# Optimization experiments

Hardware: AMD Instinct MI355X
Metric: run time of the kernel (lower is better)

Reference implementation:

```python
import jax, jax.numpy as jnp
import numpy as np

EPS = 1e-5  # nn.BatchNorm2d default eps


def _cbs(x, w, g, b, m, v):
    # Conv(k=1, bias=False) + BatchNorm2d(inference) + SiLU
    y = jnp.einsum('bchw,oc->bohw', x, w)
    s = (g * jax.lax.rsqrt(v + EPS))[None, :, None, None]
    y = (y - m[None, :, None, None]) * s + b[None, :, None, None]
    return y * jax.nn.sigmoid(y)


def setup_inputs():
    key = jax.random.key(0)
    B, D, H, W = 1, 256, 80, 80
    C = D // 2
    ks = jax.random.split(key, 20)
    r = lambda i, shape, sc=1.0: jax.random.normal(ks[i], shape, dtype=jnp.float32) * sc
    oC, oD = jnp.ones((C,), jnp.float32), jnp.ones((D,), jnp.float32)
    zC, zD = jnp.zeros((C,), jnp.float32), jnp.zeros((D,), jnp.float32)
    return {
        'x': r(0, (B, D, H, W)),
        'w1': r(1, (C, D), 0.05), 'g1': oC, 'b1': zC, 'm1': zC, 'v1': oC,
        'w2': r(2, (D, C), 0.05), 'g2': oD, 'b2': zD, 'm2': zD, 'v2': oD,
        'w3': r(3, (D, C), 0.05), 'g3': oD, 'b3': zD, 'm3': zD, 'v3': oD,
        'wq': r(4, (C, C), 0.05), 'bq': r(5, (C,), 0.01),
        'wk': r(6, (C, C), 0.05), 'bk': r(7, (C,), 0.01),
        'wv': r(8, (C, C), 0.05), 'bv': r(9, (C,), 0.01),
        'wp': r(10, (C, C), 0.05), 'bp': r(11, (C,), 0.01),
        'rel_h': r(12, (1, C, H, 1)), 'rel_w': r(13, (1, C, 1, W)),
        'ef_h': r(14, (1, C, H, 1)), 'ef_w': r(15, (1, C, 1, W)),
    }


def reference(x, w1, g1, b1, m1, v1, w2, g2, b2, m2, v2, w3, g3, b3, m3, v3,
              wq, bq, wk, bk, wv, bv, wp, bp, rel_h, rel_w, ef_h, ef_w):
    x1 = _cbs(x, w1, g1, b1, m1, v1)            # [B, C, H, W]
    B, C, H, W = x1.shape
    HW = H * W
    proj = lambda w, b: (jnp.einsum('bchw,oc->bohw', x1, w)
                         + b[None, :, None, None]).reshape(B, C, HW)
    q = proj(wq, bq)
    k = proj(wk, bk)
    v = proj(wv, bv)
    p = proj(wp, bp)
    # content-content + content-position attention branch
    cp = (rel_h + rel_w).reshape(C, HW)          # [C, HW]
    cc = jnp.einsum('bci,bcj->bij', q, k)        # [B, HW, HW]
    cpos = jnp.einsum('ci,bcj->bij', cp, q)      # [B, HW, HW]
    attn = jax.nn.softmax(cc + cpos, axis=-1)
    # out1[b,c,i] = sum_j v[b,c,j] * attn[b,i,j]  (bmm(v, attn^T))
    out1 = jnp.einsum('bcj,bij->bci', v, attn).reshape(B, C, H, W)
    # extra positional branch (valid because B == 1)
    ef = (ef_h + ef_w).reshape(B, C, HW)         # [1, C, HW]
    ce = jnp.einsum('bci,bcj->bij', p, ef)       # [B, HW, HW]
    eng = jax.nn.softmax(ce, axis=-1)
    out2 = jnp.einsum('bcj,bij->bci', ef, eng).reshape(B, C, H, W)
    return x + _cbs(out1, w2, g2, b2, m2, v2) + _cbs(out2, w3, g3, b3, m3, v3)
```

## Files before the change

kernel.cpp:

```cpp
#include <hip/hip_runtime.h>


typedef unsigned short u16;
typedef __attribute__((ext_vector_type(8))) short bf16x8;
typedef __attribute__((ext_vector_type(4))) float f32x4;
typedef __attribute__((ext_vector_type(4))) unsigned int u32x4;

#define HW 6400
#define BN_EPS 1e-5f

__device__ __forceinline__ u16 f2b(float f) {
  unsigned u = __float_as_uint(f);
  u += 0x7fffu + ((u >> 16) & 1u);
  return (u16)(u >> 16);
}
__device__ __forceinline__ unsigned pack2(float a, float b) {
  return (unsigned)f2b(a) | ((unsigned)f2b(b) << 16);
}
__device__ __forceinline__ f32x4 MFMA(bf16x8 a, bf16x8 b, f32x4 c) {
  return __builtin_amdgcn_mfma_f32_16x16x32_bf16(a, b, c, 0, 0, 0);
}
__device__ __forceinline__ float silu_f(float y) {
  return y / (1.0f + __expf(-y));
}
__device__ __forceinline__ bf16x8 pack8(f32x4 lo, f32x4 hi, float sc) {
  union { bf16x8 v; uint4 u; } r;
  r.u.x = pack2(lo[0] * sc, lo[1] * sc);
  r.u.y = pack2(lo[2] * sc, lo[3] * sc);
  r.u.z = pack2(hi[0] * sc, hi[1] * sc);
  r.u.w = pack2(hi[2] * sc, hi[3] * sc);
  return r.v;
}
__device__ __forceinline__ void gload_lds16(const u16* src, u16* dst) {
  __builtin_amdgcn_global_load_lds(
      (const __attribute__((address_space(1))) void*)src,
      (__attribute__((address_space(3))) void*)dst, 16, 0, 0);
}

__global__ void prep_all(
    const float* __restrict__ rel_h, const float* __restrict__ rel_w,
    const float* __restrict__ ef_h, const float* __restrict__ ef_w,
    const float* __restrict__ w1, const float* __restrict__ g1, const float* __restrict__ b1,
    const float* __restrict__ m1, const float* __restrict__ v1,
    const float* __restrict__ w2, const float* __restrict__ g2, const float* __restrict__ b2,
    const float* __restrict__ m2, const float* __restrict__ v2,
    const float* __restrict__ w3, const float* __restrict__ g3, const float* __restrict__ b3,
    const float* __restrict__ m3, const float* __restrict__ v3,
    const float* __restrict__ wq, const float* __restrict__ bq,
    const float* __restrict__ wk, const float* __restrict__ bk,
    const float* __restrict__ wv, const float* __restrict__ bv,
    const float* __restrict__ wp, const float* __restrict__ bp,
    u16* __restrict__ LT,
    u16* __restrict__ w1b, float* __restrict__ b1e,
    u16* __restrict__ Wcat, float* __restrict__ bcat,
    u16* __restrict__ w2b, float* __restrict__ b2e,
    u16* __restrict__ w3b, float* __restrict__ b3e,
    u16* __restrict__ efhT, u16* __restrict__ efwT,
    u16* __restrict__ efhB, u16* __restrict__ efwB,
    float* __restrict__ lbuf)
{
  const int b = blockIdx.x;
  const int t = threadIdx.x;
  if (b < 80) {
    const int h = b;
    const int c0 = (t & 63) * 2;
    const float rh0 = rel_h[c0 * 80 + h], rh1 = rel_h[(c0 + 1) * 80 + h];
    for (int wcol = (t >> 6); wcol < 80; wcol += 4) {
      const int i = h * 80 + wcol;
      float rw0 = rel_w[c0 * 80 + wcol], rw1 = rel_w[(c0 + 1) * 80 + wcol];
      *(unsigned*)&LT[(size_t)i * 256 + 128 + c0] = pack2(rh0 + rw0, rh1 + rw1);
    }
  } else if (b < 144) {
    const int tid = (b - 80) * 256 + t;
    const int stride = 64 * 256;
    for (int idx = tid; idx < 128 * 256; idx += stride) {
      int o = idx >> 8;
      float s = g1[o] * rsqrtf(v1[o] + BN_EPS);
      w1b[idx] = f2b(w1[idx] * s);
    }
    for (int idx = tid; idx < 128; idx += stride) {
      float s = g1[idx] * rsqrtf(v1[idx] + BN_EPS);
      b1e[idx] = b1[idx] - m1[idx] * s;
    }
    for (int idx = tid; idx < 4 * 128 * 128; idx += stride) {
      int which = idx >> 14, r = idx & 16383;
      const float* src = which == 0 ? wq : which == 1 ? wk : which == 2 ? wv : wp;
      Wcat[idx] = f2b(src[r]);
    }
    for (int idx = tid; idx < 512; idx += stride) {
      int which = idx >> 7, r = idx & 127;
      const float* src = which == 0 ? bq : which == 1 ? bk : which == 2 ? bv : bp;
      bcat[idx] = src[r];
    }
    for (int idx = tid; idx < 256 * 128; idx += stride) {
      int o = idx >> 7;
      float s2 = g2[o] * rsqrtf(v2[o] + BN_EPS);
      w2b[idx] = f2b(w2[idx] * s2);
      float s3 = g3[o] * rsqrtf(v3[o] + BN_EPS);
      w3b[idx] = f2b(w3[idx] * s3);
    }
    for (int idx = tid; idx < 256; idx += stride) {
      float s2 = g2[idx] * rsqrtf(v2[idx] + BN_EPS);
      b2e[idx] = b2[idx] - m2[idx] * s2;
      float s3 = g3[idx] * rsqrtf(v3[idx] + BN_EPS);
      b3e[idx] = b3[idx] - m3[idx] * s3;
    }
    for (int idx = tid; idx < 80 * 128; idx += stride) {
      int hj = idx >> 7, c = idx & 127;
      efhT[idx] = f2b(ef_h[c * 80 + hj]);
      efwT[idx] = f2b(ef_w[c * 80 + hj]);
    }
    for (int idx = tid; idx < 128 * 96; idx += stride) {
      int c = idx / 96, hj = idx % 96;
      efhB[idx] = hj < 80 ? f2b(ef_h[c * 80 + hj]) : (u16)0;
      efwB[idx] = hj < 80 ? f2b(ef_w[c * 80 + hj]) : (u16)0;
    }
  } else {
    const int tid = (b - 144) * 256 + t;
    const int stride = 32 * 256;
    for (int idx = tid; idx < HW / 4; idx += stride)
      ((f32x4*)lbuf)[idx] = (f32x4){0.f, 0.f, 0.f, 0.f};
  }
}

__global__ __launch_bounds__(256) void front_k(
    const float* __restrict__ x,
    const u16* __restrict__ w1b, const float* __restrict__ b1e,
    const u16* __restrict__ Wcat, const float* __restrict__ bcat,
    u16* __restrict__ LT, u16* __restrict__ RT, u16* __restrict__ Vv,
    u16* __restrict__ pT)
{
  __shared__ __align__(16) float xs[16][260];
  __shared__ __align__(16) u16 tr[16][136];
  const int t = threadIdx.x, lane = t & 63, w = t >> 6, jl = lane & 15, q = lane >> 4;
  const int i0 = blockIdx.x * 16;

#pragma unroll
  for (int pp = 0; pp < 4; ++pp) {
    const int p = w * 4 + pp;
    const int ch = p * 16 + (lane >> 2);
    const int ii = (lane & 3) * 4;
    f32x4 v = *(const f32x4*)(x + (size_t)ch * HW + i0 + ii);
    xs[ii][ch] = v[0]; xs[ii + 1][ch] = v[1];
    xs[ii + 2][ch] = v[2]; xs[ii + 3][ch] = v[3];
  }
  __syncthreads();

  bf16x8 afr[8];
#pragma unroll
  for (int ks = 0; ks < 8; ++ks) {
    f32x4 va = *(const f32x4*)&xs[jl][ks * 32 + q * 8];
    f32x4 vb = *(const f32x4*)&xs[jl][ks * 32 + q * 8 + 4];
    afr[ks] = pack8(va, vb, 1.0f);
  }
  f32x4 acc[2];
#pragma unroll
  for (int nn = 0; nn < 2; ++nn) acc[nn] = (f32x4){0.f, 0.f, 0.f, 0.f};
#pragma unroll
  for (int ks = 0; ks < 8; ++ks)
#pragma unroll
    for (int nn = 0; nn < 2; ++nn) {
      const int nf = w * 2 + nn;
      bf16x8 b = *(const bf16x8*)(w1b + (size_t)(nf * 16 + jl) * 256 + ks * 32 + q * 8);
      acc[nn] = MFMA(afr[ks], b, acc[nn]);
    }
#pragma unroll
  for (int nn = 0; nn < 2; ++nn) {
    const int c = (w * 2 + nn) * 16 + jl;
    const float bias = b1e[c];
#pragma unroll
    for (int r = 0; r < 4; ++r)
      tr[q * 4 + r][c] = f2b(silu_f(acc[nn][r] + bias));
  }
  __syncthreads();
  bf16x8 xa[4];
#pragma unroll
  for (int ks = 0; ks < 4; ++ks)
    xa[ks] = *(const bf16x8*)&tr[jl][ks * 32 + q * 8];

#pragma unroll
  for (int nc = 0; nc < 4; ++nc) {
    f32x4 a2[2];
#pragma unroll
    for (int nn = 0; nn < 2; ++nn) a2[nn] = (f32x4){0.f, 0.f, 0.f, 0.f};
#pragma unroll
    for (int ks = 0; ks < 4; ++ks)
#pragma unroll
      for (int nn = 0; nn < 2; ++nn) {
        const int nf = w * 2 + nn;
        bf16x8 b = *(const bf16x8*)(Wcat + (size_t)(nc * 128 + nf * 16 + jl) * 128 + ks * 32 + q * 8);
        a2[nn] = MFMA(xa[ks], b, a2[nn]);
      }
    if (nc == 2) {
#pragma unroll
      for (int nn = 0; nn < 2; ++nn) {
        const int c = (w * 2 + nn) * 16 + jl;
        const float bias = bcat[256 + c];
        uint2 pk;
        pk.x = pack2(a2[nn][0] + bias, a2[nn][1] + bias);
        pk.y = pack2(a2[nn][2] + bias, a2[nn][3] + bias);
        *(uint2*)(Vv + (size_t)c * HW + i0 + q * 4) = pk;
      }
    } else {
      __syncthreads();
#pragma unroll
      for (int nn = 0; nn < 2; ++nn) {
        const int c = (w * 2 + nn) * 16 + jl;
        const float bias = bcat[nc * 128 + c];
#pragma unroll
        for (int r = 0; r < 4; ++r)
          tr[q * 4 + r][c] = f2b(a2[nn][r] + bias);
      }
      __syncthreads();
#pragma unroll
      for (int rr = 0; rr < 4; ++rr) {
        const int r = w * 4 + rr;
        unsigned val = *(const unsigned*)&tr[r][lane * 2];
        const size_t row = (size_t)(i0 + r);
        if (nc == 0) {
          *(unsigned*)(LT + row * 256 + lane * 2) = val;
          *(unsigned*)(RT + row * 256 + 128 + lane * 2) = val;
        } else if (nc == 1) {
          *(unsigned*)(RT + row * 256 + lane * 2) = val;
        } else {
          *(unsigned*)(pT + row * 128 + lane * 2) = val;
        }
      }
    }
  }
}

__global__ __launch_bounds__(512, 2) void fused_attn(
    const u16* __restrict__ LT,
    const u16* __restrict__ RT,
    const u16* __restrict__ Vv,
    float* __restrict__ Opart,
    float* __restrict__ lv)
{
  __shared__ __align__(1024) u16 Rs[2][128 * 128];
  __shared__ __align__(1024) u16 Ts[2][64 * 128];
  const int t = threadIdx.x, lane = t & 63, w = t >> 6, jl = lane & 15, q = lane >> 4;
  const int bid = blockIdx.x;
  const int jp = bid / 50, it = bid % 50;
  const int wi = w & 1, wj = w >> 1;
  const int i0w = it * 128 + wi * 64;
  u16* Tw = Ts[wi];

  bf16x8 afr[4][8];
#pragma unroll
  for (int mt = 0; mt < 4; ++mt)
#pragma unroll
    for (int l = 0; l < 8; ++l)
      afr[mt][l] = *(const bf16x8*)(LT + (size_t)(i0w + mt * 16 + jl) * 256 + l * 32 + q * 8);

  f32x4 o[4][2];
#pragma unroll
  for (int mt = 0; mt < 4; ++mt)
#pragma unroll
    for (int cf = 0; cf < 2; ++cf) o[mt][cf] = (f32x4){0.f, 0.f, 0.f, 0.f};
  float lacc[4] = {0.f, 0.f, 0.f, 0.f};

  auto stage = [&](int jj) {
#pragma unroll
    for (int k = 0; k < 8; ++k) {
      const int b = k >> 2, cl = k & 3;
      const int cc = w * 4 + cl;
      const int jr = cc * 4 + (lane >> 4);
      const int cp = lane & 15;
      const int ch = (cp & ~7) | ((cp ^ jr) & 7);
      gload_lds16(RT + (size_t)(jj + jr) * 256 + b * 128 + ch * 8,
                  Rs[b] + (cc << 9));
    }
  };

  stage(jp * 640);

  for (int stp = 0; stp < 5; ++stp) {
    const int jj = jp * 640 + stp * 128;

    f32x4 s[2][4];
#pragma unroll
    for (int nf = 0; nf < 2; ++nf)
#pragma unroll
      for (int mt = 0; mt < 4; ++mt) s[nf][mt] = (f32x4){0.f, 0.f, 0.f, 0.f};

    __syncthreads();

#pragma unroll
    for (int h = 0; h < 2; ++h)
#pragma unroll
      for (int nf = 0; nf < 2; ++nf) {
        const int row = wj * 32 + nf * 16 + jl;
#pragma unroll
        for (int l = 0; l < 4; ++l) {
          const int ch = (l * 4 + q) ^ (jl & 7);
          bf16x8 b = *(const bf16x8*)(Rs[h] + row * 128 + ch * 8);
          s[nf][0] = MFMA(b, afr[0][h * 4 + l], s[nf][0]);
          s[nf][1] = MFMA(b, afr[1][h * 4 + l], s[nf][1]);
          s[nf][2] = MFMA(b, afr[2][h * 4 + l], s[nf][2]);
          s[nf][3] = MFMA(b, afr[3][h * 4 + l], s[nf][3]);
        }
      }
    __syncthreads();
    if (stp < 4) stage(jj + 128);

#pragma unroll
    for (int nf = 0; nf < 2; ++nf)
#pragma unroll
      for (int mt = 0; mt < 4; ++mt)
#pragma unroll
        for (int r = 0; r < 4; ++r) {
          float p = __expf(s[nf][mt][r]);
          s[nf][mt][r] = p;
          lacc[mt] += p;
        }

#pragma unroll
    for (int mt = 0; mt < 4; ++mt)
#pragma unroll
      for (int nf = 0; nf < 2; ++nf) {
        const int row = mt * 16 + jl;
        const int cs = (wj * 8 + nf * 4 + q) ^ ((jl & 7) << 2);
        uint2 pk;
        pk.x = pack2(s[nf][mt][0], s[nf][mt][1]);
        pk.y = pack2(s[nf][mt][2], s[nf][mt][3]);
        *(uint2*)(Tw + row * 128 + cs * 4) = pk;
      }
    __syncthreads();

#pragma unroll
    for (int ks2 = 0; ks2 < 4; ++ks2) {
      bf16x8 bv0 = *(const bf16x8*)(Vv + (size_t)(wj * 32 + jl) * HW + jj + ks2 * 32 + q * 8);
      bf16x8 bv1 = *(const bf16x8*)(Vv + (size_t)(wj * 32 + 16 + jl) * HW + jj + ks2 * 32 + q * 8);
      const int cb = (ks2 * 8 + q * 2) ^ ((jl & 7) << 2);
#pragma unroll
      for (int mt = 0; mt < 4; ++mt) {
        bf16x8 pa = *(const bf16x8*)(Tw + (mt * 16 + jl) * 128 + cb * 4);
        o[mt][0] = MFMA(pa, bv0, o[mt][0]);
        o[mt][1] = MFMA(pa, bv1, o[mt][1]);
      }
    }
  }

#pragma unroll
  for (int mt = 0; mt < 4; ++mt) {
    float rsum = lacc[mt];
    rsum += __shfl_xor(rsum, 16);
    rsum += __shfl_xor(rsum, 32);
    if (lane < 16)
      atomicAdd(&lv[i0w + mt * 16 + jl], rsum);
  }
#pragma unroll
  for (int mt = 0; mt < 4; ++mt) {
    const int ib = i0w + mt * 16 + q * 4;
#pragma unroll
    for (int cf = 0; cf < 2; ++cf) {
      const int c = wj * 32 + cf * 16 + jl;
#pragma unroll
      for (int r = 0; r < 4; ++r)
        Opart[((size_t)(ib + r) * 10 + jp) * 128 + c] = o[mt][cf][r];
    }
  }
}

__global__ __launch_bounds__(256) void final2(
    const u16* __restrict__ pT,
    const u16* __restrict__ efhT, const u16* __restrict__ efwT,
    const u16* __restrict__ efhB, const u16* __restrict__ efwB,
    const float* __restrict__ Opart,
    const float* __restrict__ lv,
    const u16* __restrict__ w2b, const float* __restrict__ b2e,
    const u16* __restrict__ w3b, const float* __restrict__ b3e,
    const float* __restrict__ x, float* __restrict__ outp)
{
  __shared__ __align__(16) u16 eAs[64][104];
  __shared__ __align__(16) u16 eBs[64][104];
  __shared__ float sAL[64], sBL[64];
  __shared__ __align__(16) u16 T2[64][136];
  const int t = threadIdx.x, lane = t & 63, w = t >> 6, jl = lane & 15, q = lane >> 4;
  const int i0 = blockIdx.x * 64;
  const int nc = blockIdx.y;
  const int rowA = i0 + w * 16 + jl;
  const int iloc = w * 16 + jl;

  {
    bf16x8 pfr[4];
#pragma unroll
    for (int l = 0; l < 4; ++l)
      pfr[l] = *(const bf16x8*)(pT + (size_t)rowA * 128 + l * 32 + q * 8);
    f32x4 sa[5], sb[5];
#pragma unroll
    for (int nf = 0; nf < 5; ++nf) {
      sa[nf] = (f32x4){0.f, 0.f, 0.f, 0.f};
      sb[nf] = (f32x4){0.f, 0.f, 0.f, 0.f};
    }
#pragma unroll
    for (int nf = 0; nf < 5; ++nf) {
      const int row = nf * 16 + jl;
#pragma unroll
      for (int l = 0; l < 4; ++l) {
        bf16x8 eh = *(const bf16x8*)(efhT + (size_t)row * 128 + l * 32 + q * 8);
        bf16x8 ew = *(const bf16x8*)(efwT + (size_t)row * 128 + l * 32 + q * 8);
        sa[nf] = MFMA(eh, pfr[l], sa[nf]);
        sb[nf] = MFMA(ew, pfr[l], sb[nf]);
      }
    }
    float ra = 0.f, rb = 0.f;
#pragma unroll
    for (int nf = 0; nf < 5; ++nf) {
      float ea[4], eb[4];
#pragma unroll
      for (int r = 0; r < 4; ++r) {
        ea[r] = __expf(sa[nf][r]); ra += ea[r];
        eb[r] = __expf(sb[nf][r]); rb += eb[r];
      }
      uint2 pa, pb;
      pa.x = pack2(ea[0], ea[1]); pa.y = pack2(ea[2], ea[3]);
      pb.x = pack2(eb[0], eb[1]); pb.y = pack2(eb[2], eb[3]);
      *(uint2*)&eAs[iloc][nf * 16 + q * 4] = pa;
      *(uint2*)&eBs[iloc][nf * 16 + q * 4] = pb;
    }
    *(uint2*)&eAs[iloc][80 + q * 4] = (uint2){0u, 0u};
    *(uint2*)&eBs[iloc][80 + q * 4] = (uint2){0u, 0u};
    ra += __shfl_xor(ra, 16); ra += __shfl_xor(ra, 32);
    rb += __shfl_xor(rb, 16); rb += __shfl_xor(rb, 32);
    if (lane < 16) { sAL[iloc] = ra; sBL[iloc] = rb; }
  }
  __syncthreads();

  {
    bf16x8 fa[3], fb[3];
#pragma unroll
    for (int l = 0; l < 3; ++l) {
      fa[l] = *(const bf16x8*)&eAs[iloc][l * 32 + q * 8];
      fb[l] = *(const bf16x8*)&eBs[iloc][l * 32 + q * 8];
    }
    f32x4 oU[8], oW[8];
#pragma unroll
    for (int nf = 0; nf < 8; ++nf) {
      oU[nf] = (f32x4){0.f, 0.f, 0.f, 0.f};
      oW[nf] = (f32x4){0.f, 0.f, 0.f, 0.f};
    }
#pragma unroll
    for (int l = 0; l < 3; ++l)
#pragma unroll
      for (int nf = 0; nf < 8; ++nf) {
        bf16x8 bh = *(const bf16x8*)(efhB + (size_t)(nf * 16 + jl) * 96 + l * 32 + q * 8);
        bf16x8 bw = *(const bf16x8*)(efwB + (size_t)(nf * 16 + jl) * 96 + l * 32 + q * 8);
        oU[nf] = MFMA(fa[l], bh, oU[nf]);
        oW[nf] = MFMA(fb[l], bw, oW[nf]);
      }
    float ia[4], iw[4];
#pragma unroll
    for (int r = 0; r < 4; ++r) {
      ia[r] = 1.0f / sAL[w * 16 + q * 4 + r];
      iw[r] = 1.0f / sBL[w * 16 + q * 4 + r];
    }
#pragma unroll
    for (int nf = 0; nf < 8; ++nf)
#pragma unroll
      for (int r = 0; r < 4; ++r)
        T2[w * 16 + q * 4 + r][nf * 16 + jl] =
            f2b(oU[nf][r] * ia[r] + oW[nf][r] * iw[r]);
  }
  __syncthreads();

  const float inv1 = 1.0f / lv[rowA];
  const float* OrBase = Opart + (size_t)rowA * 10 * 128;
  f32x4 a1[8], a2[8];
#pragma unroll
  for (int nf = 0; nf < 8; ++nf) {
    a1[nf] = (f32x4){0.f, 0.f, 0.f, 0.f};
    a2[nf] = (f32x4){0.f, 0.f, 0.f, 0.f};
  }
#pragma unroll
  for (int ks = 0; ks < 4; ++ks) {
    f32x4 s1a = (f32x4){0.f, 0.f, 0.f, 0.f};
    f32x4 s1b = (f32x4){0.f, 0.f, 0.f, 0.f};
#pragma unroll
    for (int p = 0; p < 10; ++p) {
      const float* Or = OrBase + p * 128;
      s1a += *(const f32x4*)(Or + ks * 32 + q * 8);
      s1b += *(const f32x4*)(Or + ks * 32 + q * 8 + 4);
    }
    bf16x8 fa1 = pack8(s1a, s1b, inv1);
    bf16x8 fa2 = *(const bf16x8*)&T2[w * 16 + jl][ks * 32 + q * 8];
#pragma unroll
    for (int nf = 0; nf < 8; ++nf) {
      bf16x8 b2f = *(const bf16x8*)(w2b + (size_t)(nc * 128 + nf * 16 + jl) * 128 + ks * 32 + q * 8);
      bf16x8 b3f = *(const bf16x8*)(w3b + (size_t)(nc * 128 + nf * 16 + jl) * 128 + ks * 32 + q * 8);
      a1[nf] = MFMA(fa1, b2f, a1[nf]);
      a2[nf] = MFMA(fa2, b3f, a2[nf]);
    }
  }
#pragma unroll
  for (int nf = 0; nf < 8; ++nf) {
    const int d = nc * 128 + nf * 16 + jl;
    const float bb2 = b2e[d], bb3 = b3e[d];
    const size_t base = (size_t)d * HW + i0 + w * 16 + q * 4;
    f32x4 xv = *(const f32x4*)(x + base);
    f32x4 rv;
#pragma unroll
    for (int r = 0; r < 4; ++r)
      rv[r] = xv[r] + silu_f(a1[nf][r] + bb2) + silu_f(a2[nf][r] + bb3);
    *(f32x4*)(outp + base) = rv;
  }
}

extern "C" void kernel_launch(void* const* d_in, const int* in_sizes, int n_in,
                              void* d_out, int out_size, void* d_ws, size_t ws_size,
                              hipStream_t stream)
{
  (void)in_sizes; (void)n_in; (void)out_size; (void)ws_size;
  const float* x   = (const float*)d_in[0];
  const float* w1  = (const float*)d_in[1];
  const float* g1  = (const float*)d_in[2];
  const float* b1  = (const float*)d_in[3];
  const float* m1  = (const float*)d_in[4];
  const float* v1  = (const float*)d_in[5];
  const float* w2  = (const float*)d_in[6];
  const float* g2  = (const float*)d_in[7];
  const float* b2  = (const float*)d_in[8];
  const float* m2  = (const float*)d_in[9];
  const float* v2  = (const float*)d_in[10];
  const float* w3  = (const float*)d_in[11];
  const float* g3  = (const float*)d_in[12];
  const float* b3  = (const float*)d_in[13];
  const float* m3  = (const float*)d_in[14];
  const float* v3  = (const float*)d_in[15];
  const float* wq  = (const float*)d_in[16];
  const float* bq  = (const float*)d_in[17];
  const float* wk  = (const float*)d_in[18];
  const float* bk  = (const float*)d_in[19];
  const float* wv  = (const float*)d_in[20];
  const float* bv  = (const float*)d_in[21];
  const float* wp  = (const float*)d_in[22];
  const float* bp  = (const float*)d_in[23];
  const float* rel_h = (const float*)d_in[24];
  const float* rel_w = (const float*)d_in[25];
  const float* ef_h  = (const float*)d_in[26];
  const float* ef_w  = (const float*)d_in[27];
  float* outp = (float*)d_out;

  char* ws = (char*)d_ws;
  size_t off = 0;
  auto alloc = [&](size_t bytes) -> void* {
    void* p = ws + off;
    off += (bytes + 511) & ~(size_t)511;
    return p;
  };
  u16* LT    = (u16*)alloc((size_t)HW * 256 * 2);
  u16* RT    = (u16*)alloc((size_t)HW * 256 * 2);
  u16* pT    = (u16*)alloc((size_t)HW * 128 * 2);
  u16* Vv    = (u16*)alloc((size_t)HW * 128 * 2);
  float* Opart = (float*)alloc((size_t)HW * 10 * 128 * 4);
  float* lbuf  = (float*)alloc((size_t)HW * 4);
  u16* w1b   = (u16*)alloc(128 * 256 * 2);
  float* b1e = (float*)alloc(128 * 4);
  u16* Wcat  = (u16*)alloc(512 * 128 * 2);
  float* bcat = (float*)alloc(512 * 4);
  u16* w2b   = (u16*)alloc(256 * 128 * 2);
  float* b2e = (float*)alloc(256 * 4);
  u16* w3b   = (u16*)alloc(256 * 128 * 2);
  float* b3e = (float*)alloc(256 * 4);
  u16* efhT  = (u16*)alloc(80 * 128 * 2);
  u16* efwT  = (u16*)alloc(80 * 128 * 2);
  u16* efhB  = (u16*)alloc(128 * 96 * 2);
  u16* efwB  = (u16*)alloc(128 * 96 * 2);

  prep_all<<<176, 256, 0, stream>>>(rel_h, rel_w, ef_h, ef_w,
                                    w1, g1, b1, m1, v1, w2, g2, b2, m2, v2,
                                    w3, g3, b3, m3, v3, wq, bq, wk, bk, wv, bv, wp, bp,
                                    LT, w1b, b1e, Wcat, bcat, w2b, b2e, w3b, b3e,
                                    efhT, efwT, efhB, efwB, lbuf);
  front_k<<<400, 256, 0, stream>>>(x, w1b, b1e, Wcat, bcat, LT, RT, Vv, pT);
  fused_attn<<<500, 512, 0, stream>>>(LT, RT, Vv, Opart, lbuf);
  final2<<<dim3(100, 2), 256, 0, stream>>>(pT, efhT, efwT, efhB, efwB,
                                           Opart, lbuf, w2b, b2e, w3b, b3e,
                                           x, outp);
}
```

Measured before the change: 240.8 us.

## Factor positional score term into separable h/w tables, halve attention K dimension

The content-position term cp^T q is split into rel_h and rel_w parts. Their products with q are precomputed in front_k as two 80xHW float tables (Ap, Bp) and added before the exp. This halves the reduction depth of the score MFMA (128 instead of 256) and halves the LT/RT storage and the RT staging traffic. Staging is also turned into true double buffering with one barrier per step. The cost is two extra fp32 table loads per score element in the attention loop and the extra table writes in front_k.

```diff
diff --git a/kernel.cpp b/kernel.cpp
--- a/kernel.cpp
+++ b/kernel.cpp
@@ -50,28 +50,19 @@
     const float* __restrict__ wk, const float* __restrict__ bk,
     const float* __restrict__ wv, const float* __restrict__ bv,
     const float* __restrict__ wp, const float* __restrict__ bp,
-    u16* __restrict__ LT,
     u16* __restrict__ w1b, float* __restrict__ b1e,
     u16* __restrict__ Wcat, float* __restrict__ bcat,
     u16* __restrict__ w2b, float* __restrict__ b2e,
     u16* __restrict__ w3b, float* __restrict__ b3e,
     u16* __restrict__ efhT, u16* __restrict__ efwT,
     u16* __restrict__ efhB, u16* __restrict__ efwB,
+    u16* __restrict__ rhT, u16* __restrict__ rwT,
     float* __restrict__ lbuf)
 {
   const int b = blockIdx.x;
   const int t = threadIdx.x;
-  if (b < 80) {
-    const int h = b;
-    const int c0 = (t & 63) * 2;
-    const float rh0 = rel_h[c0 * 80 + h], rh1 = rel_h[(c0 + 1) * 80 + h];
-    for (int wcol = (t >> 6); wcol < 80; wcol += 4) {
-      const int i = h * 80 + wcol;
-      float rw0 = rel_w[c0 * 80 + wcol], rw1 = rel_w[(c0 + 1) * 80 + wcol];
-      *(unsigned*)&LT[(size_t)i * 256 + 128 + c0] = pack2(rh0 + rw0, rh1 + rw1);
-    }
-  } else if (b < 144) {
-    const int tid = (b - 80) * 256 + t;
+  if (b < 64) {
+    const int tid = b * 256 + t;
     const int stride = 64 * 256;
     for (int idx = tid; idx < 128 * 256; idx += stride) {
       int o = idx >> 8;
@@ -109,6 +100,8 @@
       int hj = idx >> 7, c = idx & 127;
       efhT[idx] = f2b(ef_h[c * 80 + hj]);
       efwT[idx] = f2b(ef_w[c * 80 + hj]);
+      rhT[idx]  = f2b(rel_h[c * 80 + hj]);
+      rwT[idx]  = f2b(rel_w[c * 80 + hj]);
     }
     for (int idx = tid; idx < 128 * 96; idx += stride) {
       int c = idx / 96, hj = idx % 96;
@@ -116,7 +109,7 @@
       efwB[idx] = hj < 80 ? f2b(ef_w[c * 80 + hj]) : (u16)0;
     }
   } else {
-    const int tid = (b - 144) * 256 + t;
+    const int tid = (b - 64) * 256 + t;
     const int stride = 32 * 256;
     for (int idx = tid; idx < HW / 4; idx += stride)
       ((f32x4*)lbuf)[idx] = (f32x4){0.f, 0.f, 0.f, 0.f};
@@ -127,8 +120,10 @@
     const float* __restrict__ x,
     const u16* __restrict__ w1b, const float* __restrict__ b1e,
     const u16* __restrict__ Wcat, const float* __restrict__ bcat,
+    const u16* __restrict__ rhT, const u16* __restrict__ rwT,
     u16* __restrict__ LT, u16* __restrict__ RT, u16* __restrict__ Vv,
-    u16* __restrict__ pT)
+    u16* __restrict__ pT,
+    float* __restrict__ Ap, float* __restrict__ Bp)
 {
   __shared__ __align__(16) float xs[16][260];
   __shared__ __align__(16) u16 tr[16][136];
@@ -218,12 +213,34 @@
         unsigned val = *(const unsigned*)&tr[r][lane * 2];
         const size_t row = (size_t)(i0 + r);
         if (nc == 0) {
-          *(unsigned*)(LT + row * 256 + lane * 2) = val;
-          *(unsigned*)(RT + row * 256 + 128 + lane * 2) = val;
+          *(unsigned*)(LT + row * 128 + lane * 2) = val;
         } else if (nc == 1) {
-          *(unsigned*)(RT + row * 256 + lane * 2) = val;
+          *(unsigned*)(RT + row * 128 + lane * 2) = val;
         } else {
           *(unsigned*)(pT + row * 128 + lane * 2) = val;
+        }
+      }
+      if (nc == 0) {
+        bf16x8 qf[4];
+#pragma unroll
+        for (int ks = 0; ks < 4; ++ks)
+          qf[ks] = *(const bf16x8*)&tr[jl][ks * 32 + q * 8];
+        for (int nf = w; nf < 5; nf += 4) {
+          f32x4 aa = (f32x4){0.f, 0.f, 0.f, 0.f};
+          f32x4 bb = (f32x4){0.f, 0.f, 0.f, 0.f};
+#pragma unroll
+          for (int ks = 0; ks < 4; ++ks) {
+            bf16x8 rh = *(const bf16x8*)(rhT + (size_t)(nf * 16 + jl) * 128 + ks * 32 + q * 8);
+            bf16x8 rw = *(const bf16x8*)(rwT + (size_t)(nf * 16 + jl) * 128 + ks * 32 + q * 8);
+            aa = MFMA(rh, qf[ks], aa);
+            bb = MFMA(rw, qf[ks], bb);
+          }
+#pragma unroll
+          for (int r = 0; r < 4; ++r) {
+            const int h = nf * 16 + q * 4 + r;
+            Ap[(size_t)h * HW + i0 + jl] = aa[r];
+            Bp[(size_t)h * HW + i0 + jl] = bb[r];
+          }
         }
       }
     }
@@ -234,6 +251,8 @@
     const u16* __restrict__ LT,
     const u16* __restrict__ RT,
     const u16* __restrict__ Vv,
+    const float* __restrict__ Ap,
+    const float* __restrict__ Bp,
     float* __restrict__ Opart,
     float* __restrict__ lv)
 {
@@ -246,12 +265,21 @@
   const int i0w = it * 128 + wi * 64;
   u16* Tw = Ts[wi];
 
-  bf16x8 afr[4][8];
+  bf16x8 afr[4][4];
 #pragma unroll
   for (int mt = 0; mt < 4; ++mt)
 #pragma unroll
-    for (int l = 0; l < 8; ++l)
-      afr[mt][l] = *(const bf16x8*)(LT + (size_t)(i0w + mt * 16 + jl) * 256 + l * 32 + q * 8);
+    for (int l = 0; l < 4; ++l)
+      afr[mt][l] = *(const bf16x8*)(LT + (size_t)(i0w + mt * 16 + jl) * 128 + l * 32 + q * 8);
+
+  const float* Arow[4];
+  const float* Brow[4];
+#pragma unroll
+  for (int mt = 0; mt < 4; ++mt) {
+    const int i = i0w + mt * 16 + jl;
+    Arow[mt] = Ap + (size_t)(i / 80) * HW;
+    Brow[mt] = Bp + (size_t)(i % 80) * HW;
+  }
 
   f32x4 o[4][2];
 #pragma unroll
@@ -260,20 +288,20 @@
     for (int cf = 0; cf < 2; ++cf) o[mt][cf] = (f32x4){0.f, 0.f, 0.f, 0.f};
   float lacc[4] = {0.f, 0.f, 0.f, 0.f};
 
-  auto stage = [&](int jj) {
-#pragma unroll
-    for (int k = 0; k < 8; ++k) {
-      const int b = k >> 2, cl = k & 3;
-      const int cc = w * 4 + cl;
+  auto stage = [&](int jj, int buf) {
+#pragma unroll
+    for (int k = 0; k < 4; ++k) {
+      const int cc = w * 4 + k;
       const int jr = cc * 4 + (lane >> 4);
       const int cp = lane & 15;
       const int ch = (cp & ~7) | ((cp ^ jr) & 7);
-      gload_lds16(RT + (size_t)(jj + jr) * 256 + b * 128 + ch * 8,
-                  Rs[b] + (cc << 9));
+      gload_lds16(RT + (size_t)(jj + jr) * 128 + ch * 8,
+                  Rs[buf] + (cc << 9));
     }
   };
 
-  stage(jp * 640);
+  stage(jp * 640, 0);
+  int cur = 0;
 
   for (int stp = 0; stp < 5; ++stp) {
     const int jj = jp * 640 + stp * 128;
@@ -285,35 +313,37 @@
       for (int mt = 0; mt < 4; ++mt) s[nf][mt] = (f32x4){0.f, 0.f, 0.f, 0.f};
 
     __syncthreads();
-
-#pragma unroll
-    for (int h = 0; h < 2; ++h)
-#pragma unroll
-      for (int nf = 0; nf < 2; ++nf) {
-        const int row = wj * 32 + nf * 16 + jl;
-#pragma unroll
-        for (int l = 0; l < 4; ++l) {
-          const int ch = (l * 4 + q) ^ (jl & 7);
-          bf16x8 b = *(const bf16x8*)(Rs[h] + row * 128 + ch * 8);
-          s[nf][0] = MFMA(b, afr[0][h * 4 + l], s[nf][0]);
-          s[nf][1] = MFMA(b, afr[1][h * 4 + l], s[nf][1]);
-          s[nf][2] = MFMA(b, afr[2][h * 4 + l], s[nf][2]);
-          s[nf][3] = MFMA(b, afr[3][h * 4 + l], s[nf][3]);
-        }
-      }
-    __syncthreads();
-    if (stp < 4) stage(jj + 128);
-
-#pragma unroll
-    for (int nf = 0; nf < 2; ++nf)
-#pragma unroll
-      for (int mt = 0; mt < 4; ++mt)
+    if (stp < 4) stage(jj + 128, cur ^ 1);
+
+#pragma unroll
+    for (int nf = 0; nf < 2; ++nf) {
+      const int row = wj * 32 + nf * 16 + jl;
+#pragma unroll
+      for (int l = 0; l < 4; ++l) {
+        const int ch = (l * 4 + q) ^ (jl & 7);
+        bf16x8 b = *(const bf16x8*)(Rs[cur] + row * 128 + ch * 8);
+        s[nf][0] = MFMA(b, afr[0][l], s[nf][0]);
+        s[nf][1] = MFMA(b, afr[1][l], s[nf][1]);
+        s[nf][2] = MFMA(b, afr[2][l], s[nf][2]);
+        s[nf][3] = MFMA(b, afr[3][l], s[nf][3]);
+      }
+    }
+
+#pragma unroll
+    for (int nf = 0; nf < 2; ++nf) {
+      const int jcol = jj + wj * 32 + nf * 16 + q * 4;
+#pragma unroll
+      for (int mt = 0; mt < 4; ++mt) {
+        f32x4 av = *(const f32x4*)(Arow[mt] + jcol);
+        f32x4 bv = *(const f32x4*)(Brow[mt] + jcol);
 #pragma unroll
         for (int r = 0; r < 4; ++r) {
-          float p = __expf(s[nf][mt][r]);
+          float p = __expf(s[nf][mt][r] + av[r] + bv[r]);
           s[nf][mt][r] = p;
           lacc[mt] += p;
         }
+      }
+    }
 
 #pragma unroll
     for (int mt = 0; mt < 4; ++mt)
@@ -340,6 +370,7 @@
         o[mt][1] = MFMA(pa, bv1, o[mt][1]);
       }
     }
+    cur ^= 1;
   }
 
 #pragma unroll
@@ -549,12 +580,14 @@
     off += (bytes + 511) & ~(size_t)511;
     return p;
   };
-  u16* LT    = (u16*)alloc((size_t)HW * 256 * 2);
-  u16* RT    = (u16*)alloc((size_t)HW * 256 * 2);
+  u16* LT    = (u16*)alloc((size_t)HW * 128 * 2);
+  u16* RT    = (u16*)alloc((size_t)HW * 128 * 2);
   u16* pT    = (u16*)alloc((size_t)HW * 128 * 2);
   u16* Vv    = (u16*)alloc((size_t)HW * 128 * 2);
   float* Opart = (float*)alloc((size_t)HW * 10 * 128 * 4);
   float* lbuf  = (float*)alloc((size_t)HW * 4);
+  float* Ap  = (float*)alloc((size_t)80 * HW * 4);
+  float* Bp  = (float*)alloc((size_t)80 * HW * 4);
   u16* w1b   = (u16*)alloc(128 * 256 * 2);
   float* b1e = (float*)alloc(128 * 4);
   u16* Wcat  = (u16*)alloc(512 * 128 * 2);
@@ -567,14 +600,17 @@
   u16* efwT  = (u16*)alloc(80 * 128 * 2);
   u16* efhB  = (u16*)alloc(128 * 96 * 2);
   u16* efwB  = (u16*)alloc(128 * 96 * 2);
-
-  prep_all<<<176, 256, 0, stream>>>(rel_h, rel_w, ef_h, ef_w,
-                                    w1, g1, b1, m1, v1, w2, g2, b2, m2, v2,
-                                    w3, g3, b3, m3, v3, wq, bq, wk, bk, wv, bv, wp, bp,
-                                    LT, w1b, b1e, Wcat, bcat, w2b, b2e, w3b, b3e,
-                                    efhT, efwT, efhB, efwB, lbuf);
-  front_k<<<400, 256, 0, stream>>>(x, w1b, b1e, Wcat, bcat, LT, RT, Vv, pT);
-  fused_attn<<<500, 512, 0, stream>>>(LT, RT, Vv, Opart, lbuf);
+  u16* rhT   = (u16*)alloc(80 * 128 * 2);
+  u16* rwT   = (u16*)alloc(80 * 128 * 2);
+
+  prep_all<<<96, 256, 0, stream>>>(rel_h, rel_w, ef_h, ef_w,
+                                   w1, g1, b1, m1, v1, w2, g2, b2, m2, v2,
+                                   w3, g3, b3, m3, v3, wq, bq, wk, bk, wv, bv, wp, bp,
+                                   w1b, b1e, Wcat, bcat, w2b, b2e, w3b, b3e,
+                                   efhT, efwT, efhB, efwB, rhT, rwT, lbuf);
+  front_k<<<400, 256, 0, stream>>>(x, w1b, b1e, Wcat, bcat, rhT, rwT,
+                                   LT, RT, Vv, pT, Ap, Bp);
+  fused_attn<<<500, 512, 0, stream>>>(LT, RT, Vv, Ap, Bp, Opart, lbuf);
   final2<<<dim3(100, 2), 256, 0, stream>>>(pT, efhT, efwT, efhB, efwB,
                                            Opart, lbuf, w2b, b2e, w3b, b3e,
                                            x, outp);
```

Result: no change. 245.1 us (+1.8%).
